# Kernel optimization log

Measured on AMD Instinct MI355X. Metric: run time of the kernel, lower is better.

## Reference

```python
import jax, jax.numpy as jnp
import numpy as np

B, T, E = 2, 2048, 1024
H, Dh = 16, 64  # num_heads, head_size; H*Dh == E


def setup_inputs() -> dict:
    key = jax.random.key(0)
    ks = jax.random.split(key, 5)
    s = 0.02
    return {
        "x": jax.random.normal(ks[0], (B, T, E), dtype=jnp.float32),
        "Wq": jax.random.normal(ks[1], (E, H * Dh), dtype=jnp.float32) * s,
        "Wk": jax.random.normal(ks[2], (E, H * Dh), dtype=jnp.float32) * s,
        "Wv": jax.random.normal(ks[3], (E, H * Dh), dtype=jnp.float32) * s,
        "Wo": jax.random.normal(ks[4], (H * Dh, E), dtype=jnp.float32) * s,
        "bo": jnp.zeros((E,), dtype=jnp.float32),
    }


def reference(x, Wq, Wk, Wv, Wo, bo):
    # Batched equivalent of the per-head Python loop: each head's bias-free
    # q/k/v Linear is one column-block of Wq/Wk/Wv.
    b, t, e = x.shape
    q = (x @ Wq).reshape(b, t, H, Dh)  # [B,T,H,Dh]
    k = (x @ Wk).reshape(b, t, H, Dh)
    v = (x @ Wv).reshape(b, t, H, Dh)

    scale = 1.0 / jnp.sqrt(jnp.asarray(Dh, dtype=x.dtype))
    scores = jnp.einsum("bqhd,bkhd->bhqk", q, k) * scale  # [B,H,T,T]
    causal = jnp.tril(jnp.ones((t, t), dtype=bool))
    scores = jnp.where(causal[None, None, :, :], scores, jnp.asarray(-jnp.inf, dtype=x.dtype))
    attn = jax.nn.softmax(scores, axis=-1)

    out = jnp.einsum("bhqk,bkhd->bqhd", attn, v).reshape(b, t, H * Dh)  # concat heads
    return out @ Wo + bo  # output projection (dropout is identity at p=0)
```

## Files before the change

### kernel.cpp

```cpp
#include <hip/hip_runtime.h>
#include <hip/hip_bf16.h>

typedef __attribute__((ext_vector_type(8))) short bf16x8;
typedef __attribute__((ext_vector_type(4))) float f32x4;
typedef __attribute__((ext_vector_type(4))) unsigned short u16x4;

__device__ __forceinline__ unsigned short f2bf(float f) {
    union { float f; unsigned int i; } x; x.f = f;
    unsigned int lsb = (x.i >> 16) & 1u;
    x.i += 0x7fffu + lsb;
    return (unsigned short)(x.i >> 16);
}

__device__ __forceinline__ void gl_lds16(const unsigned short* g, unsigned short* l) {
    __builtin_amdgcn_global_load_lds(
        (const __attribute__((address_space(1))) void*)g,
        (__attribute__((address_space(3))) void*)l, 16, 0, 0);
}

__device__ __forceinline__ unsigned int cvt_pk_bf16(float lo, float hi) {
    unsigned int d;
    asm("v_cvt_pk_bf16_f32 %0, %1, %2" : "=v"(d) : "v"(lo), "v"(hi));
    return d;
}

__device__ __forceinline__ bf16x8 pf_build_s(f32x4 pa, f32x4 pb, float s) {
    unsigned int E0 = cvt_pk_bf16(pa[0] * s, pa[1] * s);
    unsigned int O0 = cvt_pk_bf16(pa[2] * s, pa[3] * s);
    unsigned int E1 = cvt_pk_bf16(pb[0] * s, pb[1] * s);
    unsigned int O1 = cvt_pk_bf16(pb[2] * s, pb[3] * s);
    asm("v_permlane32_swap_b32 %0, %1" : "+v"(E0), "+v"(E1));
    asm("v_permlane32_swap_b32 %0, %1" : "+v"(O0), "+v"(O1));
    asm("v_permlane16_swap_b32 %0, %1" : "+v"(E0), "+v"(E1));
    asm("v_permlane16_swap_b32 %0, %1" : "+v"(O0), "+v"(O1));
    union { unsigned int u[4]; bf16x8 v; } r;
    r.u[0] = E0; r.u[1] = O0; r.u[2] = E1; r.u[3] = O1;
    return r.v;
}

__global__ __launch_bounds__(256) void prep(
    const float* __restrict__ x,
    const float* __restrict__ Wq, const float* __restrict__ Wk,
    const float* __restrict__ Wv, const float* __restrict__ Wo,
    unsigned short* __restrict__ xb,
    unsigned short* __restrict__ WqkvT, unsigned short* __restrict__ WoT)
{
    const int E = 1024;
    const int bid = blockIdx.x;
    __shared__ float t[32][33];

    if (bid < 4096) {
        int i = bid * 256 + threadIdx.x;
        f32x4 v = ((const f32x4*)x)[i];
        u16x4 o;
#pragma unroll
        for (int j = 0; j < 4; ++j) o[j] = f2bf(v[j]);
        ((u16x4*)xb)[i] = o;
        return;
    }
    const int r = bid - 4096;
    const int which = r >> 10;
    const int sub = r & 1023;
    const float* src = which == 0 ? Wq : which == 1 ? Wk : which == 2 ? Wv : Wo;
    unsigned short* dst = which == 3 ? WoT : WqkvT + (size_t)which * E * E;

    const int tx = threadIdx.x & 31, ty = threadIdx.x >> 5;
    const int n0 = (sub & 31) * 32, k0 = (sub >> 5) * 32;
#pragma unroll
    for (int i = 0; i < 4; ++i)
        t[ty + 8 * i][tx] = src[(size_t)(k0 + ty + 8 * i) * E + n0 + tx];
    __syncthreads();
#pragma unroll
    for (int i = 0; i < 4; ++i)
        dst[(size_t)(n0 + ty + 8 * i) * E + k0 + tx] = f2bf(t[tx][ty + 8 * i]);
}

template <int PERM>
__global__ __launch_bounds__(256) void gemm128(
    const unsigned short* __restrict__ A,
    const unsigned short* __restrict__ BT,
    const float* __restrict__ bias,
    float* __restrict__ Cf,
    unsigned short* __restrict__ q_out,
    unsigned short* __restrict__ k_out,
    unsigned short* __restrict__ v_out,
    int M, int N, int K)
{
    __shared__ __align__(16) unsigned short As[128 * 32];
    __shared__ __align__(16) unsigned short Bs[128 * 32];

    const int tid  = threadIdx.x;
    const int wave = tid >> 6;
    const int lane = tid & 63;
    const int ln15 = lane & 15;
    const int kg   = lane >> 4;
    const int bm = blockIdx.x * 128, bn = blockIdx.y * 128;
    const int wm = (wave >> 1) * 64, wn = (wave & 1) * 64;

    f32x4 acc[4][4];
#pragma unroll
    for (int i = 0; i < 4; ++i)
#pragma unroll
        for (int j = 0; j < 4; ++j) acc[i][j] = (f32x4){0.f, 0.f, 0.f, 0.f};

    const int sr = wave * 32 + (lane >> 2);
    const int sc = (lane & 3) * 8;

    for (int k0 = 0; k0 < K; k0 += 32) {
        gl_lds16(A  + (size_t)(bm + sr)      * K + k0 + sc, As + wave * 1024);
        gl_lds16(A  + (size_t)(bm + sr + 16) * K + k0 + sc, As + wave * 1024 + 512);
        gl_lds16(BT + (size_t)(bn + sr)      * K + k0 + sc, Bs + wave * 1024);
        gl_lds16(BT + (size_t)(bn + sr + 16) * K + k0 + sc, Bs + wave * 1024 + 512);
        __syncthreads();

        bf16x8 af[4], bw[4];
#pragma unroll
        for (int mt = 0; mt < 4; ++mt)
            af[mt] = *(const bf16x8*)&As[(wm + mt * 16 + ln15) * 32 + kg * 8];
#pragma unroll
        for (int nt = 0; nt < 4; ++nt)
            bw[nt] = *(const bf16x8*)&Bs[(wn + nt * 16 + ln15) * 32 + kg * 8];
        if (PERM == 0) {
#pragma unroll
            for (int mt = 0; mt < 4; ++mt)
#pragma unroll
                for (int nt = 0; nt < 4; ++nt)
                    acc[mt][nt] = __builtin_amdgcn_mfma_f32_16x16x32_bf16(
                        bw[nt], af[mt], acc[mt][nt], 0, 0, 0);
        } else {
#pragma unroll
            for (int mt = 0; mt < 4; ++mt)
#pragma unroll
                for (int nt = 0; nt < 4; ++nt)
                    acc[mt][nt] = __builtin_amdgcn_mfma_f32_16x16x32_bf16(
                        af[mt], bw[nt], acc[mt][nt], 0, 0, 0);
        }
        __syncthreads();
    }

    if (PERM == 0) {
#pragma unroll
        for (int mt = 0; mt < 4; ++mt) {
            const int row = bm + wm + mt * 16 + ln15;
#pragma unroll
            for (int nt = 0; nt < 4; ++nt) {
                const int c0 = bn + wn + nt * 16 + kg * 4;
                f32x4 bv = *(const f32x4*)(bias + c0);
                f32x4 o;
#pragma unroll
                for (int r = 0; r < 4; ++r) o[r] = acc[mt][nt][r] + bv[r];
                *(f32x4*)(Cf + (size_t)row * N + c0) = o;
            }
        }
    } else {
        const int sec = bn >> 10;
        if (sec < 2) {
            unsigned short* dst = sec == 0 ? q_out : k_out;
            const float scale = sec == 0 ? 0.125f : 1.0f;
#pragma unroll
            for (int nt = 0; nt < 4; ++nt) {
                const int col = bn + wn + nt * 16 + ln15;
                const int h = (col >> 6) & 15, d = col & 63;
#pragma unroll
                for (int mt = 0; mt < 4; ++mt) {
#pragma unroll
                    for (int r = 0; r < 4; ++r) {
                        const int row = bm + wm + mt * 16 + kg * 4 + r;
                        const int b = row >> 11, t = row & 2047;
                        dst[((size_t)(b * 16 + h) * 2048 + t) * 64 + d] =
                            f2bf(acc[mt][nt][r] * scale);
                    }
                }
            }
        } else {
#pragma unroll
            for (int nt = 0; nt < 4; ++nt) {
                const int c = bn + wn + nt * 16 + ln15;
                const int h = (c >> 6) & 15, d = c & 63;
#pragma unroll
                for (int mp = 0; mp < 2; ++mp) {
                    const int t0 = bm + wm + mp * 32 + kg * 8;
                    const int b = t0 >> 11, t = t0 & 2047;
                    bf16x8 pf = pf_build_s(acc[2 * mp][nt], acc[2 * mp + 1][nt], 1.0f);
                    *(bf16x8*)(v_out + ((size_t)(b * 16 + h) * 64 + d) * 2048 + t) = pf;
                }
            }
        }
    }
}

__device__ __forceinline__ void softmax_tile(
    f32x4 sr[4], bool diag, int q_loc, int kg,
    bf16x8& pf0, bf16x8& pf1, f32x4& accl, bf16x8 ones)
{
    if (diag) {
#pragma unroll
        for (int kt = 0; kt < 4; ++kt)
#pragma unroll
            for (int r = 0; r < 4; ++r)
                if (kt * 16 + kg * 4 + r > q_loc) sr[kt][r] = -1e30f;
    }
    f32x4 pe[4];
#pragma unroll
    for (int kt = 0; kt < 4; ++kt)
#pragma unroll
        for (int r = 0; r < 4; ++r) pe[kt][r] = __expf(sr[kt][r]);
    pf0 = pf_build_s(pe[0], pe[1], 1.0f);
    pf1 = pf_build_s(pe[2], pe[3], 1.0f);
    accl = __builtin_amdgcn_mfma_f32_16x16x32_bf16(pf0, ones, accl, 0, 0, 0);
    accl = __builtin_amdgcn_mfma_f32_16x16x32_bf16(pf1, ones, accl, 0, 0, 0);
}

__global__ __launch_bounds__(256) void flash_attn(
    const unsigned short* __restrict__ Q,
    const unsigned short* __restrict__ Km,
    const unsigned short* __restrict__ Vtg,
    unsigned short* __restrict__ O,
    int T, int H)
{
    __shared__ __align__(16) unsigned short Ks[2][64][72];
    __shared__ __align__(16) unsigned short Vs[2][64][72];

    const int tid  = threadIdx.x;
    const int wave = tid >> 6;
    const int lane = tid & 63;
    const int ln15 = lane & 15;
    const int kg   = lane >> 4;
    const int sA   = blockIdx.x;
    const int sB   = (T >> 6) - 1 - sA;
    const int kmax = sB;
    const int bh   = blockIdx.y;
    const int b    = bh >> 4, h = bh & 15;
    const size_t base  = (size_t)bh * T * 64;
    const size_t vbase = (size_t)bh * 64 * T;
    const int q_loc = wave * 16 + ln15;

    bf16x8 qf[2][2];
    {
        const unsigned short* QrA = Q + base + (size_t)(sA * 64 + q_loc) * 64;
        const unsigned short* QrB = Q + base + (size_t)(sB * 64 + q_loc) * 64;
        qf[0][0] = *(const bf16x8*)(QrA + kg * 8);
        qf[0][1] = *(const bf16x8*)(QrA + 32 + kg * 8);
        qf[1][0] = *(const bf16x8*)(QrB + kg * 8);
        qf[1][1] = *(const bf16x8*)(QrB + 32 + kg * 8);
    }

    bf16x8 ones;
    {
        const short o = (ln15 == 0) ? (short)0x3F80 : (short)0;
#pragma unroll
        for (int j = 0; j < 8; ++j) ones[j] = o;
    }

    f32x4 o_acc[2][4];
#pragma unroll
    for (int s = 0; s < 2; ++s)
#pragma unroll
        for (int dt = 0; dt < 4; ++dt) o_acc[s][dt] = (f32x4){0.f, 0.f, 0.f, 0.f};
    f32x4 acc_l[2] = {(f32x4){0.f, 0.f, 0.f, 0.f}, (f32x4){0.f, 0.f, 0.f, 0.f}};

    const int sky = tid >> 3;
    const int sd  = (tid & 7) * 8;

    bf16x8 pk0, pk1, pv0, pv1;
    pk0 = *(const bf16x8*)(Km + base + (size_t)sky * 64 + sd);
    pk1 = *(const bf16x8*)(Km + base + (size_t)(sky + 32) * 64 + sd);
    pv0 = *(const bf16x8*)(Vtg + vbase + (size_t)sky * T + sd);
    pv1 = *(const bf16x8*)(Vtg + vbase + (size_t)(sky + 32) * T + sd);

    for (int kb = 0; kb <= kmax; ++kb) {
        const int bufi = kb & 1;
        *(bf16x8*)&Ks[bufi][sky][sd]      = pk0;
        *(bf16x8*)&Ks[bufi][sky + 32][sd] = pk1;
        *(bf16x8*)&Vs[bufi][sky][sd]      = pv0;
        *(bf16x8*)&Vs[bufi][sky + 32][sd] = pv1;
        if (kb < kmax) {
            const int kn = (kb + 1) * 64;
            pk0 = *(const bf16x8*)(Km + base + (size_t)(kn + sky) * 64 + sd);
            pk1 = *(const bf16x8*)(Km + base + (size_t)(kn + sky + 32) * 64 + sd);
            pv0 = *(const bf16x8*)(Vtg + vbase + (size_t)sky * T + kn + sd);
            pv1 = *(const bf16x8*)(Vtg + vbase + (size_t)(sky + 32) * T + kn + sd);
        }
        __syncthreads();

        const bool doA = (kb <= sA);

        f32x4 srB[4], srA[4];
#pragma unroll
        for (int kt = 0; kt < 4; ++kt) {
            bf16x8 kf0 = *(const bf16x8*)&Ks[bufi][kt * 16 + ln15][kg * 8];
            bf16x8 kf1 = *(const bf16x8*)&Ks[bufi][kt * 16 + ln15][32 + kg * 8];
            f32x4 a = (f32x4){0.f, 0.f, 0.f, 0.f};
            a = __builtin_amdgcn_mfma_f32_16x16x32_bf16(kf0, qf[1][0], a, 0, 0, 0);
            a = __builtin_amdgcn_mfma_f32_16x16x32_bf16(kf1, qf[1][1], a, 0, 0, 0);
            srB[kt] = a;
            if (doA) {
                f32x4 c = (f32x4){0.f, 0.f, 0.f, 0.f};
                c = __builtin_amdgcn_mfma_f32_16x16x32_bf16(kf0, qf[0][0], c, 0, 0, 0);
                c = __builtin_amdgcn_mfma_f32_16x16x32_bf16(kf1, qf[0][1], c, 0, 0, 0);
                srA[kt] = c;
            }
        }

        bf16x8 pfB0, pfB1, pfA0, pfA1;
        softmax_tile(srB, kb == sB, q_loc, kg, pfB0, pfB1, acc_l[1], ones);
        if (doA)
            softmax_tile(srA, kb == sA, q_loc, kg, pfA0, pfA1, acc_l[0], ones);

#pragma unroll
        for (int dt = 0; dt < 4; ++dt) {
            bf16x8 vf0 = *(const bf16x8*)&Vs[bufi][dt * 16 + ln15][kg * 8];
            bf16x8 vf1 = *(const bf16x8*)&Vs[bufi][dt * 16 + ln15][32 + kg * 8];
            o_acc[1][dt] = __builtin_amdgcn_mfma_f32_16x16x32_bf16(pfB0, vf0, o_acc[1][dt], 0, 0, 0);
            o_acc[1][dt] = __builtin_amdgcn_mfma_f32_16x16x32_bf16(pfB1, vf1, o_acc[1][dt], 0, 0, 0);
            if (doA) {
                o_acc[0][dt] = __builtin_amdgcn_mfma_f32_16x16x32_bf16(pfA0, vf0, o_acc[0][dt], 0, 0, 0);
                o_acc[0][dt] = __builtin_amdgcn_mfma_f32_16x16x32_bf16(pfA1, vf1, o_acc[0][dt], 0, 0, 0);
            }
        }
    }

#pragma unroll
    for (int s = 0; s < 2; ++s) {
        const int qb = (s == 0 ? sA : sB) * 64;
        float inv[4];
#pragma unroll
        for (int r = 0; r < 4; ++r)
            inv[r] = 1.0f / __shfl(acc_l[s][r], lane & 48, 64);
#pragma unroll
        for (int dt = 0; dt < 4; ++dt)
#pragma unroll
            for (int r = 0; r < 4; ++r) {
                const int t = qb + wave * 16 + kg * 4 + r;
                const int d = dt * 16 + ln15;
                O[(size_t)(b * T + t) * (H * 64) + h * 64 + d] =
                    f2bf(o_acc[s][dt][r] * inv[r]);
            }
    }
}

extern "C" void kernel_launch(void* const* d_in, const int* in_sizes, int n_in,
                              void* d_out, int out_size, void* d_ws, size_t ws_size,
                              hipStream_t stream)
{
    const int B = 2, T = 2048, E = 1024, H = 16;
    const int M = B * T;

    const float* x  = (const float*)d_in[0];
    const float* Wq = (const float*)d_in[1];
    const float* Wk = (const float*)d_in[2];
    const float* Wv = (const float*)d_in[3];
    const float* Wo = (const float*)d_in[4];
    const float* bo = (const float*)d_in[5];
    float* out = (float*)d_out;

    unsigned short* xb     = (unsigned short*)d_ws;
    unsigned short* WqkvT  = xb + (size_t)M * E;
    unsigned short* WoT    = WqkvT + (size_t)3 * E * E;
    unsigned short* q      = WoT + (size_t)E * E;
    unsigned short* k      = q + (size_t)M * E;
    unsigned short* vT     = k + (size_t)M * E;
    unsigned short* ao     = vT + (size_t)M * E;

    prep<<<8192, 256, 0, stream>>>(x, Wq, Wk, Wv, Wo, xb, WqkvT, WoT);

    dim3 g1(M / 128, 3 * E / 128);
    gemm128<1><<<g1, 256, 0, stream>>>(xb, WqkvT, nullptr, nullptr, q, k, vT,
                                       M, 3 * E, E);

    dim3 ag(T / 128, B * H);
    flash_attn<<<ag, 256, 0, stream>>>(q, k, vT, ao, T, H);

    dim3 g2(M / 128, E / 128);
    gemm128<0><<<g2, 256, 0, stream>>>(ao, WoT, bo, out, nullptr, nullptr, nullptr,
                                       M, E, E);
}
```

Measured before the change: 185.2 us.

## Load K/V fragments directly from global memory instead of staging through LDS

Removes the double-buffered shared-memory staging of K and V tiles, along with the per-iteration block barrier. Each wave now loads its MFMA operand fragments straight from global memory, relying on L1/L2 caching because all four waves read the same tiles. It also wraps the MFMA sections in s_setprio to raise wave priority during matrix work. In exchange it loses the register prefetch overlap, exposes global load latency inside the loop, and sends redundant per-wave reads through the cache.

```diff
diff --git a/kernel.cpp b/kernel.cpp
--- a/kernel.cpp
+++ b/kernel.cpp
@@ -218,9 +218,6 @@
     unsigned short* __restrict__ O,
     int T, int H)
 {
-    __shared__ __align__(16) unsigned short Ks[2][64][72];
-    __shared__ __align__(16) unsigned short Vs[2][64][72];
-
     const int tid  = threadIdx.x;
     const int wave = tid >> 6;
     const int lane = tid & 63;
@@ -259,37 +256,20 @@
         for (int dt = 0; dt < 4; ++dt) o_acc[s][dt] = (f32x4){0.f, 0.f, 0.f, 0.f};
     f32x4 acc_l[2] = {(f32x4){0.f, 0.f, 0.f, 0.f}, (f32x4){0.f, 0.f, 0.f, 0.f}};
 
-    const int sky = tid >> 3;
-    const int sd  = (tid & 7) * 8;
-
-    bf16x8 pk0, pk1, pv0, pv1;
-    pk0 = *(const bf16x8*)(Km + base + (size_t)sky * 64 + sd);
-    pk1 = *(const bf16x8*)(Km + base + (size_t)(sky + 32) * 64 + sd);
-    pv0 = *(const bf16x8*)(Vtg + vbase + (size_t)sky * T + sd);
-    pv1 = *(const bf16x8*)(Vtg + vbase + (size_t)(sky + 32) * T + sd);
+    const unsigned short* Kl = Km + base + (size_t)ln15 * 64 + kg * 8;
+    const unsigned short* Vl = Vtg + vbase + (size_t)ln15 * T + kg * 8;
 
     for (int kb = 0; kb <= kmax; ++kb) {
-        const int bufi = kb & 1;
-        *(bf16x8*)&Ks[bufi][sky][sd]      = pk0;
-        *(bf16x8*)&Ks[bufi][sky + 32][sd] = pk1;
-        *(bf16x8*)&Vs[bufi][sky][sd]      = pv0;
-        *(bf16x8*)&Vs[bufi][sky + 32][sd] = pv1;
-        if (kb < kmax) {
-            const int kn = (kb + 1) * 64;
-            pk0 = *(const bf16x8*)(Km + base + (size_t)(kn + sky) * 64 + sd);
-            pk1 = *(const bf16x8*)(Km + base + (size_t)(kn + sky + 32) * 64 + sd);
-            pv0 = *(const bf16x8*)(Vtg + vbase + (size_t)sky * T + kn + sd);
-            pv1 = *(const bf16x8*)(Vtg + vbase + (size_t)(sky + 32) * T + kn + sd);
-        }
-        __syncthreads();
-
+        const int k0 = kb * 64;
         const bool doA = (kb <= sA);
 
         f32x4 srB[4], srA[4];
+        __builtin_amdgcn_s_setprio(1);
 #pragma unroll
         for (int kt = 0; kt < 4; ++kt) {
-            bf16x8 kf0 = *(const bf16x8*)&Ks[bufi][kt * 16 + ln15][kg * 8];
-            bf16x8 kf1 = *(const bf16x8*)&Ks[bufi][kt * 16 + ln15][32 + kg * 8];
+            const unsigned short* kp = Kl + (size_t)(k0 + kt * 16) * 64;
+            bf16x8 kf0 = *(const bf16x8*)(kp);
+            bf16x8 kf1 = *(const bf16x8*)(kp + 32);
             f32x4 a = (f32x4){0.f, 0.f, 0.f, 0.f};
             a = __builtin_amdgcn_mfma_f32_16x16x32_bf16(kf0, qf[1][0], a, 0, 0, 0);
             a = __builtin_amdgcn_mfma_f32_16x16x32_bf16(kf1, qf[1][1], a, 0, 0, 0);
@@ -301,16 +281,19 @@
                 srA[kt] = c;
             }
         }
+        __builtin_amdgcn_s_setprio(0);
 
         bf16x8 pfB0, pfB1, pfA0, pfA1;
         softmax_tile(srB, kb == sB, q_loc, kg, pfB0, pfB1, acc_l[1], ones);
         if (doA)
             softmax_tile(srA, kb == sA, q_loc, kg, pfA0, pfA1, acc_l[0], ones);
 
+        __builtin_amdgcn_s_setprio(1);
 #pragma unroll
         for (int dt = 0; dt < 4; ++dt) {
-            bf16x8 vf0 = *(const bf16x8*)&Vs[bufi][dt * 16 + ln15][kg * 8];
-            bf16x8 vf1 = *(const bf16x8*)&Vs[bufi][dt * 16 + ln15][32 + kg * 8];
+            const unsigned short* vp = Vl + (size_t)(dt * 16) * T + k0;
+            bf16x8 vf0 = *(const bf16x8*)(vp);
+            bf16x8 vf1 = *(const bf16x8*)(vp + 32);
             o_acc[1][dt] = __builtin_amdgcn_mfma_f32_16x16x32_bf16(pfB0, vf0, o_acc[1][dt], 0, 0, 0);
             o_acc[1][dt] = __builtin_amdgcn_mfma_f32_16x16x32_bf16(pfB1, vf1, o_acc[1][dt], 0, 0, 0);
             if (doA) {
@@ -318,6 +301,7 @@
                 o_acc[0][dt] = __builtin_amdgcn_mfma_f32_16x16x32_bf16(pfA1, vf1, o_acc[0][dt], 0, 0, 0);
             }
         }
+        __builtin_amdgcn_s_setprio(0);
     }
 
 #pragma unroll
```

Measured after the change: 264.3 us. 42.7% more time.

## Replace paired causal q-block scheduling with one q-block per workgroup

Applied to the files above, without the earlier changes.

The attention kernel stops pairing a short and a long causal query block in each workgroup and instead gives each workgroup a single 64-row query block, doubling the grid. Blocks are issued in descending work order so the longest ones start first. This removes the doA branching and halves the accumulator registers, which may raise occupancy. The cost is that every K/V tile is loaded from global memory and staged in LDS for one query block instead of two, and per-block work is less even.

```diff
diff --git a/kernel.cpp b/kernel.cpp
--- a/kernel.cpp
+++ b/kernel.cpp
@@ -226,23 +226,19 @@
     const int lane = tid & 63;
     const int ln15 = lane & 15;
     const int kg   = lane >> 4;
-    const int sA   = blockIdx.x;
-    const int sB   = (T >> 6) - 1 - sA;
-    const int kmax = sB;
+    const int s    = (T >> 6) - 1 - blockIdx.x;
+    const int kmax = s;
     const int bh   = blockIdx.y;
     const int b    = bh >> 4, h = bh & 15;
     const size_t base  = (size_t)bh * T * 64;
     const size_t vbase = (size_t)bh * 64 * T;
     const int q_loc = wave * 16 + ln15;
 
-    bf16x8 qf[2][2];
+    bf16x8 qf[2];
     {
-        const unsigned short* QrA = Q + base + (size_t)(sA * 64 + q_loc) * 64;
-        const unsigned short* QrB = Q + base + (size_t)(sB * 64 + q_loc) * 64;
-        qf[0][0] = *(const bf16x8*)(QrA + kg * 8);
-        qf[0][1] = *(const bf16x8*)(QrA + 32 + kg * 8);
-        qf[1][0] = *(const bf16x8*)(QrB + kg * 8);
-        qf[1][1] = *(const bf16x8*)(QrB + 32 + kg * 8);
+        const unsigned short* Qr = Q + base + (size_t)(s * 64 + q_loc) * 64;
+        qf[0] = *(const bf16x8*)(Qr + kg * 8);
+        qf[1] = *(const bf16x8*)(Qr + 32 + kg * 8);
     }
 
     bf16x8 ones;
@@ -252,12 +248,10 @@
         for (int j = 0; j < 8; ++j) ones[j] = o;
     }
 
-    f32x4 o_acc[2][4];
-#pragma unroll
-    for (int s = 0; s < 2; ++s)
-#pragma unroll
-        for (int dt = 0; dt < 4; ++dt) o_acc[s][dt] = (f32x4){0.f, 0.f, 0.f, 0.f};
-    f32x4 acc_l[2] = {(f32x4){0.f, 0.f, 0.f, 0.f}, (f32x4){0.f, 0.f, 0.f, 0.f}};
+    f32x4 o_acc[4];
+#pragma unroll
+    for (int dt = 0; dt < 4; ++dt) o_acc[dt] = (f32x4){0.f, 0.f, 0.f, 0.f};
+    f32x4 acc_l = (f32x4){0.f, 0.f, 0.f, 0.f};
 
     const int sky = tid >> 3;
     const int sd  = (tid & 7) * 8;
@@ -283,60 +277,42 @@
         }
         __syncthreads();
 
-        const bool doA = (kb <= sA);
-
-        f32x4 srB[4], srA[4];
+        f32x4 sr[4];
 #pragma unroll
         for (int kt = 0; kt < 4; ++kt) {
             bf16x8 kf0 = *(const bf16x8*)&Ks[bufi][kt * 16 + ln15][kg * 8];
             bf16x8 kf1 = *(const bf16x8*)&Ks[bufi][kt * 16 + ln15][32 + kg * 8];
             f32x4 a = (f32x4){0.f, 0.f, 0.f, 0.f};
-            a = __builtin_amdgcn_mfma_f32_16x16x32_bf16(kf0, qf[1][0], a, 0, 0, 0);
-            a = __builtin_amdgcn_mfma_f32_16x16x32_bf16(kf1, qf[1][1], a, 0, 0, 0);
-            srB[kt] = a;
-            if (doA) {
-                f32x4 c = (f32x4){0.f, 0.f, 0.f, 0.f};
-                c = __builtin_amdgcn_mfma_f32_16x16x32_bf16(kf0, qf[0][0], c, 0, 0, 0);
-                c = __builtin_amdgcn_mfma_f32_16x16x32_bf16(kf1, qf[0][1], c, 0, 0, 0);
-                srA[kt] = c;
-            }
-        }
-
-        bf16x8 pfB0, pfB1, pfA0, pfA1;
-        softmax_tile(srB, kb == sB, q_loc, kg, pfB0, pfB1, acc_l[1], ones);
-        if (doA)
-            softmax_tile(srA, kb == sA, q_loc, kg, pfA0, pfA1, acc_l[0], ones);
+            a = __builtin_amdgcn_mfma_f32_16x16x32_bf16(kf0, qf[0], a, 0, 0, 0);
+            a = __builtin_amdgcn_mfma_f32_16x16x32_bf16(kf1, qf[1], a, 0, 0, 0);
+            sr[kt] = a;
+        }
+
+        bf16x8 pf0, pf1;
+        softmax_tile(sr, kb == kmax, q_loc, kg, pf0, pf1, acc_l, ones);
 
 #pragma unroll
         for (int dt = 0; dt < 4; ++dt) {
             bf16x8 vf0 = *(const bf16x8*)&Vs[bufi][dt * 16 + ln15][kg * 8];
             bf16x8 vf1 = *(const bf16x8*)&Vs[bufi][dt * 16 + ln15][32 + kg * 8];
-            o_acc[1][dt] = __builtin_amdgcn_mfma_f32_16x16x32_bf16(pfB0, vf0, o_acc[1][dt], 0, 0, 0);
-            o_acc[1][dt] = __builtin_amdgcn_mfma_f32_16x16x32_bf16(pfB1, vf1, o_acc[1][dt], 0, 0, 0);
-            if (doA) {
-                o_acc[0][dt] = __builtin_amdgcn_mfma_f32_16x16x32_bf16(pfA0, vf0, o_acc[0][dt], 0, 0, 0);
-                o_acc[0][dt] = __builtin_amdgcn_mfma_f32_16x16x32_bf16(pfA1, vf1, o_acc[0][dt], 0, 0, 0);
-            }
-        }
-    }
-
-#pragma unroll
-    for (int s = 0; s < 2; ++s) {
-        const int qb = (s == 0 ? sA : sB) * 64;
-        float inv[4];
-#pragma unroll
-        for (int r = 0; r < 4; ++r)
-            inv[r] = 1.0f / __shfl(acc_l[s][r], lane & 48, 64);
-#pragma unroll
-        for (int dt = 0; dt < 4; ++dt)
-#pragma unroll
-            for (int r = 0; r < 4; ++r) {
-                const int t = qb + wave * 16 + kg * 4 + r;
-                const int d = dt * 16 + ln15;
-                O[(size_t)(b * T + t) * (H * 64) + h * 64 + d] =
-                    f2bf(o_acc[s][dt][r] * inv[r]);
-            }
-    }
+            o_acc[dt] = __builtin_amdgcn_mfma_f32_16x16x32_bf16(pf0, vf0, o_acc[dt], 0, 0, 0);
+            o_acc[dt] = __builtin_amdgcn_mfma_f32_16x16x32_bf16(pf1, vf1, o_acc[dt], 0, 0, 0);
+        }
+    }
+
+    float inv[4];
+#pragma unroll
+    for (int r = 0; r < 4; ++r)
+        inv[r] = 1.0f / __shfl(acc_l[r], lane & 48, 64);
+#pragma unroll
+    for (int dt = 0; dt < 4; ++dt)
+#pragma unroll
+        for (int r = 0; r < 4; ++r) {
+            const int t = s * 64 + wave * 16 + kg * 4 + r;
+            const int d = dt * 16 + ln15;
+            O[(size_t)(b * T + t) * (H * 64) + h * 64 + d] =
+                f2bf(o_acc[dt][r] * inv[r]);
+        }
 }
 
 extern "C" void kernel_launch(void* const* d_in, const int* in_sizes, int n_in,
@@ -368,7 +344,7 @@
     gemm128<1><<<g1, 256, 0, stream>>>(xb, WqkvT, nullptr, nullptr, q, k, vT,
                                        M, 3 * E, E);
 
-    dim3 ag(T / 128, B * H);
+    dim3 ag(T / 64, B * H);
     flash_attn<<<ag, 256, 0, stream>>>(q, k, vT, ao, T, H);
 
     dim3 g2(M / 128, E / 128);
```

Result: slower. 198.9 us (+7.4%).
